# Optimization experiments

Measured on AMD Instinct MI355X. Metric: run time of the kernel, lower is better.

Reference implementation:

```python
import jax, jax.numpy as jnp
import numpy as np

B, C, E = 4, 2048, 1024
H, D = 16, 64

def setup_inputs() -> dict:
    key = jax.random.key(0)
    kx, kq, kk, kv, ko = jax.random.split(key, 5)
    s = 1.0 / np.sqrt(E)
    return {
        "x": jax.random.normal(kx, (B, C, E), dtype=jnp.float32),
        "W_q": jax.random.uniform(kq, (E, H * D), jnp.float32, -s, s),
        "W_k": jax.random.uniform(kk, (E, H * D), jnp.float32, -s, s),
        "W_v": jax.random.uniform(kv, (E, H * D), jnp.float32, -s, s),
        "W_o": jax.random.uniform(ko, (H * D, E), jnp.float32, -s, s),
    }

def reference(x, W_q, W_k, W_v, W_o):
    b, c, e = x.shape
    # project and split heads: [B, H, C, D]
    q = (x @ W_q).reshape(b, c, H, D).transpose(0, 2, 1, 3)
    k = (x @ W_k).reshape(b, c, H, D).transpose(0, 2, 1, 3)
    v = (x @ W_v).reshape(b, c, H, D).transpose(0, 2, 1, 3)
    scores = jnp.einsum('bhqd,bhkd->bhqk', q, k) / jnp.sqrt(jnp.float32(D))
    causal = jnp.tril(jnp.ones((c, c), dtype=bool))
    scores = jnp.where(causal, scores, -jnp.inf)
    weights = jax.nn.softmax(scores, axis=-1)
    hidden = jnp.einsum('bhqk,bhkd->bhqd', weights, v)
    hidden = hidden.transpose(0, 2, 1, 3).reshape(b, c, H * D)
    return hidden @ W_o
```

## Files before the change

### kernel.cpp

```cpp
#include <hip/hip_runtime.h>
#include <hip/hip_bf16.h>


typedef __attribute__((ext_vector_type(8))) short short8;
typedef __attribute__((ext_vector_type(4))) float floatx4;
typedef __attribute__((ext_vector_type(4))) unsigned short ushort4v;

__device__ __forceinline__ unsigned short f2bf(float f) {
    __hip_bfloat16 h = __float2bfloat16(f);
    return __builtin_bit_cast(unsigned short, h);
}

__device__ __forceinline__ void gl2lds16(const unsigned short* g, unsigned short* l) {
    __builtin_amdgcn_global_load_lds(
        (const __attribute__((address_space(1))) unsigned int*)g,
        (__attribute__((address_space(3))) unsigned int*)l, 16, 0, 0);
}

__global__ __launch_bounds__(256) void prep_kernel(const float* __restrict__ x,
                                                   const float* __restrict__ W0,
                                                   const float* __restrict__ W1,
                                                   const float* __restrict__ W2,
                                                   const float* __restrict__ W3,
                                                   unsigned short* __restrict__ xb,
                                                   unsigned short* __restrict__ wt) {
    __shared__ float tile[64][65];
    const int id = blockIdx.x;
    if (id < 8192) {
        const int i = id * 256 + threadIdx.x;
        const float4 v = ((const float4*)x)[i];
        ushort4v o;
        o[0] = f2bf(v.x); o[1] = f2bf(v.y); o[2] = f2bf(v.z); o[3] = f2bf(v.w);
        ((ushort4v*)xb)[i] = o;
        return;
    }
    const int t2 = id - 8192;
    const int z = t2 >> 8;
    const float* src = (z == 0) ? W0 : (z == 1) ? W1 : (z == 2) ? W2 : W3;
    const float scale = (z == 0) ? 0.18033688011112042f : 1.0f;
    unsigned short* dst = wt + (size_t)z * 1048576;
    const int k0 = ((t2 >> 4) & 15) * 64, n0 = (t2 & 15) * 64;
    const int t = threadIdx.x;
    const int r = t >> 4, c4 = (t & 15) * 4;
    #pragma unroll
    for (int p = 0; p < 4; ++p) {
        const int kk = p * 16 + r;
        const float4 v = *(const float4*)&src[(size_t)(k0 + kk) * 1024 + n0 + c4];
        tile[kk][c4 + 0] = v.x; tile[kk][c4 + 1] = v.y;
        tile[kk][c4 + 2] = v.z; tile[kk][c4 + 3] = v.w;
    }
    __syncthreads();
    #pragma unroll
    for (int p = 0; p < 4; ++p) {
        const int nn = p * 16 + r;
        ushort4v o;
        #pragma unroll
        for (int j = 0; j < 4; ++j) o[j] = f2bf(tile[c4 + j][nn] * scale);
        *(ushort4v*)&dst[(size_t)(n0 + nn) * 1024 + k0 + c4] = o;
    }
}

template<int MODE, int NBLK>
__global__ __launch_bounds__(256) void gemm128(const unsigned short* __restrict__ A,
                                               const unsigned short* __restrict__ Bt,
                                               unsigned short* __restrict__ obf,
                                               float* __restrict__ ofp) {
    constexpr int Kd = 1024;
    __shared__ __align__(16) unsigned short Al[128 * 64];
    __shared__ __align__(16) unsigned short Bl[128 * 64];
    const int id = blockIdx.x;
    const int xcd = id & 7;
    const int q = id >> 3;
    const int m_blk = xcd * 8 + (q & 7);
    const int n_blk = q >> 3;
    const int m0 = m_blk * 128, n0 = n_blk * 128;

    const int tid = threadIdx.x;
    const int lane = tid & 63, w = tid >> 6;
    const int quad = lane >> 4, l15 = lane & 15;
    const int wm = (w & 1) * 64, wn = (w >> 1) * 64;
    const int srow = lane >> 3, sc = lane & 7;
    const int gc = (sc ^ srow) * 8;

    floatx4 acc[4][4];
    #pragma unroll
    for (int i = 0; i < 4; ++i)
        #pragma unroll
        for (int j = 0; j < 4; ++j) acc[i][j] = (floatx4){0.f, 0.f, 0.f, 0.f};

    for (int kt = 0; kt < Kd / 64; ++kt) {
        const int k0 = kt * 64;
        #pragma unroll
        for (int p = 0; p < 4; ++p) {
            const int row0 = w * 32 + p * 8;
            gl2lds16(&A[(size_t)(m0 + row0 + srow) * Kd + k0 + gc], &Al[row0 * 64]);
            gl2lds16(&Bt[(size_t)(n0 + row0 + srow) * Kd + k0 + gc], &Bl[row0 * 64]);
        }
        __syncthreads();
        #pragma unroll
        for (int kk = 0; kk < 2; ++kk) {
            short8 af[4], bfv[4];
            #pragma unroll
            for (int i = 0; i < 4; ++i) {
                const int row = wm + i * 16 + l15;
                af[i] = *(const short8*)&Al[row * 64 + ((kk * 4 + quad) ^ (row & 7)) * 8];
            }
            #pragma unroll
            for (int i = 0; i < 4; ++i) {
                const int row = wn + i * 16 + l15;
                bfv[i] = *(const short8*)&Bl[row * 64 + ((kk * 4 + quad) ^ (row & 7)) * 8];
            }
            #pragma unroll
            for (int i = 0; i < 4; ++i)
                #pragma unroll
                for (int j = 0; j < 4; ++j)
                    acc[i][j] = __builtin_amdgcn_mfma_f32_16x16x32_bf16(
                        af[i], bfv[j], acc[i][j], 0, 0, 0);
        }
        __syncthreads();
    }

    #pragma unroll
    for (int i = 0; i < 4; ++i) {
        if (MODE == 0 && n0 >= 2048) {
            #pragma unroll
            for (int j = 0; j < 4; ++j) {
                const int mb = m0 + wm + i * 16 + quad * 4;
                const int n = n0 + wn + j * 16 + l15;
                const int b = mb >> 11, c0 = mb & 2047;
                const int nl = n & 1023, hh = nl >> 6, d = nl & 63;
                ushort4v pv;
                #pragma unroll
                for (int r = 0; r < 4; ++r) pv[r] = f2bf(acc[i][j][r]);
                *(ushort4v*)&obf[16777216 + ((size_t)(b * 16 + hh) * 64 + d) * 2048 + c0] = pv;
            }
        } else {
            #pragma unroll
            for (int r = 0; r < 4; ++r) {
                const int m = m0 + wm + i * 16 + quad * 4 + r;
                #pragma unroll
                for (int j = 0; j < 4; ++j) {
                    const int n = n0 + wn + j * 16 + l15;
                    const float v = acc[i][j][r];
                    if (MODE == 0) {
                        const int b = m >> 11, c = m & 2047;
                        const int z = n >> 10, nl = n & 1023, hh = nl >> 6, d = nl & 63;
                        obf[(size_t)z * 8388608 +
                            ((size_t)(b * 16 + hh) * 2048 + c) * 64 + d] = f2bf(v);
                    } else {
                        ofp[(size_t)m * 1024 + n] = v;
                    }
                }
            }
        }
    }
}

__global__ __launch_bounds__(512) void attn_kernel(const unsigned short* __restrict__ Q,
                                                   const unsigned short* __restrict__ K,
                                                   const unsigned short* __restrict__ Vt,
                                                   unsigned short* __restrict__ Hid) {
    __shared__ __align__(16) unsigned short Kl[2][64 * 64];
    __shared__ __align__(16) unsigned short Vl[2][64 * 64];
    __shared__ __align__(16) unsigned short Pl[8][16 * 72];
    const int id = blockIdx.x;
    const int bh = (id >> 6) * 8 + (id & 7);
    const int xq = (id >> 3) & 7;
    const int b = bh >> 4, h = bh & 15;
    const int tid = threadIdx.x, w = tid >> 6, lane = tid & 63;
    const int quad = lane >> 4, l15 = lane & 15;
    const int sw = quad ^ (l15 & 7);
    const int srow = lane >> 3, sc = lane & 7;
    const int g8 = (sc ^ srow) * 8;
    const int krow = w * 8 + srow;
    const size_t bhs = (size_t)(b * 16 + h) * 2048 * 64;
    const unsigned short* Qb = Q + bhs;
    const unsigned short* Kb = K + bhs;
    const unsigned short* Vb = Vt + bhs;

    #pragma unroll
    for (int pass = 0; pass < 2; ++pass) {
        const int qt = pass ? (15 - xq) : xq;
        const int q0 = qt * 128;
        const int qw = q0 + w * 16;
        const int myq = qw + l15;
        const short8 bq0 = *(const short8*)&Qb[(size_t)myq * 64 + quad * 8];
        const short8 bq1 = *(const short8*)&Qb[(size_t)myq * 64 + 32 + quad * 8];

        floatx4 o[4];
        #pragma unroll
        for (int i = 0; i < 4; ++i) o[i] = (floatx4){0.f, 0.f, 0.f, 0.f};
        float li = 0.f;

        const int nT = (q0 + 128) >> 6;
        __syncthreads();
        gl2lds16(&Kb[(size_t)krow * 64 + g8], &Kl[0][w * 512]);
        gl2lds16(&Vb[(size_t)krow * 2048 + g8], &Vl[0][w * 512]);

        for (int t = 0; t < nT; ++t) {
            const int k0 = t * 64;
            const int cb = t & 1;
            __syncthreads();
            if (t + 1 < nT) {
                const int kn = k0 + 64;
                gl2lds16(&Kb[(size_t)(kn + krow) * 64 + g8], &Kl[cb ^ 1][w * 512]);
                gl2lds16(&Vb[(size_t)krow * 2048 + kn + g8], &Vl[cb ^ 1][w * 512]);
            }
            if (k0 <= qw + 15) {
                floatx4 s[4];
                #pragma unroll
                for (int kf = 0; kf < 4; ++kf) {
                    const int row = kf * 16 + l15;
                    const short8 ka0 = *(const short8*)&Kl[cb][row * 64 + sw * 8];
                    const short8 ka1 = *(const short8*)&Kl[cb][row * 64 + (sw ^ 4) * 8];
                    floatx4 ss = (floatx4){0.f, 0.f, 0.f, 0.f};
                    ss = __builtin_amdgcn_mfma_f32_16x16x32_bf16(ka0, bq0, ss, 0, 0, 0);
                    ss = __builtin_amdgcn_mfma_f32_16x16x32_bf16(ka1, bq1, ss, 0, 0, 0);
                    s[kf] = ss;
                }
                if (k0 + 63 > qw) {
                    #pragma unroll
                    for (int kf = 0; kf < 4; ++kf) {
                        ushort4v pw;
                        #pragma unroll
                        for (int r = 0; r < 4; ++r) {
                            const int key = k0 + kf * 16 + quad * 4 + r;
                            const float p = (key > myq) ? 0.f
                                            : __builtin_amdgcn_exp2f(s[kf][r]);
                            li += p;
                            pw[r] = f2bf(p);
                        }
                        *(ushort4v*)&Pl[w][l15 * 72 + kf * 16 + quad * 4] = pw;
                    }
                } else {
                    #pragma unroll
                    for (int kf = 0; kf < 4; ++kf) {
                        ushort4v pw;
                        #pragma unroll
                        for (int r = 0; r < 4; ++r) {
                            const float p = __builtin_amdgcn_exp2f(s[kf][r]);
                            li += p;
                            pw[r] = f2bf(p);
                        }
                        *(ushort4v*)&Pl[w][l15 * 72 + kf * 16 + quad * 4] = pw;
                    }
                }
                __threadfence_block();
                const short8 pb0 = *(const short8*)&Pl[w][l15 * 72 + quad * 8];
                const short8 pb1 = *(const short8*)&Pl[w][l15 * 72 + 32 + quad * 8];
                #pragma unroll
                for (int nt = 0; nt < 4; ++nt) {
                    const int row = nt * 16 + l15;
                    const short8 va0 = *(const short8*)&Vl[cb][row * 64 + sw * 8];
                    const short8 va1 = *(const short8*)&Vl[cb][row * 64 + (sw ^ 4) * 8];
                    floatx4 oo = o[nt];
                    oo = __builtin_amdgcn_mfma_f32_16x16x32_bf16(va0, pb0, oo, 0, 0, 0);
                    oo = __builtin_amdgcn_mfma_f32_16x16x32_bf16(va1, pb1, oo, 0, 0, 0);
                    o[nt] = oo;
                }
            }
        }

        li += __shfl_xor(li, 16, 64);
        li += __shfl_xor(li, 32, 64);
        const float inv = 1.f / li;
        #pragma unroll
        for (int nt = 0; nt < 4; ++nt) {
            ushort4v ov;
            #pragma unroll
            for (int r = 0; r < 4; ++r) ov[r] = f2bf(o[nt][r] * inv);
            *(ushort4v*)&Hid[((size_t)b * 2048 + myq) * 1024 + h * 64 + nt * 16 + quad * 4] = ov;
        }
    }
}

extern "C" void kernel_launch(void* const* d_in, const int* in_sizes, int n_in,
                              void* d_out, int out_size, void* d_ws, size_t ws_size,
                              hipStream_t stream) {
    const float* x  = (const float*)d_in[0];
    const float* Wq = (const float*)d_in[1];
    const float* Wk = (const float*)d_in[2];
    const float* Wv = (const float*)d_in[3];
    const float* Wo = (const float*)d_in[4];
    float* out = (float*)d_out;
    unsigned short* ws = (unsigned short*)d_ws;

    const size_t XB  = 0;
    const size_t WQT = 8388608;
    const size_t QO  = 12582912;
    const size_t HO  = 37748736;

    prep_kernel<<<9216, 256, 0, stream>>>(x, Wq, Wk, Wv, Wo, ws + XB, ws + WQT);

    gemm128<0, 24><<<1536, 256, 0, stream>>>(ws + XB, ws + WQT, ws + QO, nullptr);
    attn_kernel<<<512, 512, 0, stream>>>(ws + QO, ws + QO + 8388608,
                                         ws + QO + 16777216, ws + HO);
    gemm128<1, 8><<<512, 256, 0, stream>>>(ws + HO, ws + WQT + 3145728, nullptr, out);
}
```

Measured before the change: 232.9 us.

## Use 256x256 double-buffered tiles for the QKV projection GEMM

Replaces the 128x128 QKV GEMM with a dedicated 512-thread kernel that computes 256x256 output tiles, with 8 waves each holding 128x64 accumulators. It double-buffers the LDS tiles so the next K-slice loads while MFMAs run on the current one, with one barrier per step. The larger tile raises arithmetic intensity and cuts global traffic, and the prefetch hides load latency. In exchange it uses more registers and 128KB of LDS per block, and launches only 384 blocks, which may leave CUs underused. The output projection is split into its own specialised kernel without the mode template.

```diff
diff --git a/kernel.cpp b/kernel.cpp
--- a/kernel.cpp
+++ b/kernel.cpp
@@ -60,11 +60,110 @@
     }
 }
 
-template<int MODE, int NBLK>
-__global__ __launch_bounds__(256) void gemm128(const unsigned short* __restrict__ A,
-                                               const unsigned short* __restrict__ Bt,
-                                               unsigned short* __restrict__ obf,
-                                               float* __restrict__ ofp) {
+__global__ __launch_bounds__(512, 2) void gemmqkv(const unsigned short* __restrict__ A,
+                                                  const unsigned short* __restrict__ Bt,
+                                                  unsigned short* __restrict__ obf) {
+    constexpr int Kd = 1024;
+    __shared__ __align__(16) unsigned short Al[2][256 * 64];
+    __shared__ __align__(16) unsigned short Bl[2][256 * 64];
+    const int id = blockIdx.x;
+    const int xcd = id & 7;
+    const int idx = id >> 3;
+    const int m_blk = xcd * 4 + (idx & 3);
+    const int n_blk = idx >> 2;
+    const int m0 = m_blk * 256, n0 = n_blk * 256;
+
+    const int tid = threadIdx.x;
+    const int lane = tid & 63, w = tid >> 6;
+    const int quad = lane >> 4, l15 = lane & 15;
+    const int wm = (w & 1) * 128, wn = (w >> 1) * 64;
+    const int srow = lane >> 3, sc = lane & 7;
+    const int gc = (sc ^ srow) * 8;
+
+    floatx4 acc[8][4];
+    #pragma unroll
+    for (int i = 0; i < 8; ++i)
+        #pragma unroll
+        for (int j = 0; j < 4; ++j) acc[i][j] = (floatx4){0.f, 0.f, 0.f, 0.f};
+
+    #pragma unroll
+    for (int p = 0; p < 4; ++p) {
+        const int row0 = w * 32 + p * 8;
+        gl2lds16(&A[(size_t)(m0 + row0 + srow) * Kd + gc], &Al[0][row0 * 64]);
+        gl2lds16(&Bt[(size_t)(n0 + row0 + srow) * Kd + gc], &Bl[0][row0 * 64]);
+    }
+
+    for (int kt = 0; kt < 16; ++kt) {
+        const int cb = kt & 1;
+        __syncthreads();
+        if (kt < 15) {
+            const int kn = kt * 64 + 64;
+            #pragma unroll
+            for (int p = 0; p < 4; ++p) {
+                const int row0 = w * 32 + p * 8;
+                gl2lds16(&A[(size_t)(m0 + row0 + srow) * Kd + kn + gc],
+                         &Al[cb ^ 1][row0 * 64]);
+                gl2lds16(&Bt[(size_t)(n0 + row0 + srow) * Kd + kn + gc],
+                         &Bl[cb ^ 1][row0 * 64]);
+            }
+        }
+        #pragma unroll
+        for (int kk = 0; kk < 2; ++kk) {
+            short8 af[8], bfv[4];
+            #pragma unroll
+            for (int j = 0; j < 4; ++j) {
+                const int row = wn + j * 16 + l15;
+                bfv[j] = *(const short8*)&Bl[cb][row * 64 + ((kk * 4 + quad) ^ (row & 7)) * 8];
+            }
+            #pragma unroll
+            for (int i = 0; i < 8; ++i) {
+                const int row = wm + i * 16 + l15;
+                af[i] = *(const short8*)&Al[cb][row * 64 + ((kk * 4 + quad) ^ (row & 7)) * 8];
+            }
+            #pragma unroll
+            for (int i = 0; i < 8; ++i)
+                #pragma unroll
+                for (int j = 0; j < 4; ++j)
+                    acc[i][j] = __builtin_amdgcn_mfma_f32_16x16x32_bf16(
+                        af[i], bfv[j], acc[i][j], 0, 0, 0);
+        }
+    }
+
+    if (n0 >= 2048) {
+        #pragma unroll
+        for (int i = 0; i < 8; ++i)
+            #pragma unroll
+            for (int j = 0; j < 4; ++j) {
+                const int mb = m0 + wm + i * 16 + quad * 4;
+                const int n = n0 + wn + j * 16 + l15;
+                const int b = mb >> 11, c0 = mb & 2047;
+                const int nl = n & 1023, hh = nl >> 6, d = nl & 63;
+                ushort4v pv;
+                #pragma unroll
+                for (int r = 0; r < 4; ++r) pv[r] = f2bf(acc[i][j][r]);
+                *(ushort4v*)&obf[16777216 + ((size_t)(b * 16 + hh) * 64 + d) * 2048 + c0] = pv;
+            }
+    } else {
+        #pragma unroll
+        for (int i = 0; i < 8; ++i)
+            #pragma unroll
+            for (int r = 0; r < 4; ++r) {
+                const int m = m0 + wm + i * 16 + quad * 4 + r;
+                const int b = m >> 11, c = m & 2047;
+                #pragma unroll
+                for (int j = 0; j < 4; ++j) {
+                    const int n = n0 + wn + j * 16 + l15;
+                    const int z = n >> 10, nl = n & 1023, hh = nl >> 6, d = nl & 63;
+                    obf[(size_t)z * 8388608 +
+                        ((size_t)(b * 16 + hh) * 2048 + c) * 64 + d] = f2bf(acc[i][j][r]);
+                }
+            }
+    }
+}
+
+__global__ __launch_bounds__(256) void gemmproj(const unsigned short* __restrict__ A,
+                                                const unsigned short* __restrict__ Bt,
+                                                float* __restrict__ ofp) {
     constexpr int Kd = 1024;
     __shared__ __align__(16) unsigned short Al[128 * 64];
     __shared__ __align__(16) unsigned short Bl[128 * 64];
@@ -121,39 +220,14 @@
     }
 
     #pragma unroll
-    for (int i = 0; i < 4; ++i) {
-        if (MODE == 0 && n0 >= 2048) {
-            #pragma unroll
-            for (int j = 0; j < 4; ++j) {
-                const int mb = m0 + wm + i * 16 + quad * 4;
-                const int n = n0 + wn + j * 16 + l15;
-                const int b = mb >> 11, c0 = mb & 2047;
-                const int nl = n & 1023, hh = nl >> 6, d = nl & 63;
-                ushort4v pv;
-                #pragma unroll
-                for (int r = 0; r < 4; ++r) pv[r] = f2bf(acc[i][j][r]);
-                *(ushort4v*)&obf[16777216 + ((size_t)(b * 16 + hh) * 64 + d) * 2048 + c0] = pv;
-            }
-        } else {
-            #pragma unroll
-            for (int r = 0; r < 4; ++r) {
-                const int m = m0 + wm + i * 16 + quad * 4 + r;
-                #pragma unroll
-                for (int j = 0; j < 4; ++j) {
-                    const int n = n0 + wn + j * 16 + l15;
-                    const float v = acc[i][j][r];
-                    if (MODE == 0) {
-                        const int b = m >> 11, c = m & 2047;
-                        const int z = n >> 10, nl = n & 1023, hh = nl >> 6, d = nl & 63;
-                        obf[(size_t)z * 8388608 +
-                            ((size_t)(b * 16 + hh) * 2048 + c) * 64 + d] = f2bf(v);
-                    } else {
-                        ofp[(size_t)m * 1024 + n] = v;
-                    }
-                }
-            }
-        }
-    }
+    for (int i = 0; i < 4; ++i)
+        #pragma unroll
+        for (int r = 0; r < 4; ++r) {
+            const int m = m0 + wm + i * 16 + quad * 4 + r;
+            #pragma unroll
+            for (int j = 0; j < 4; ++j)
+                ofp[(size_t)m * 1024 + n0 + wn + j * 16 + l15] = acc[i][j][r];
+        }
 }
 
 __global__ __launch_bounds__(512) void attn_kernel(const unsigned short* __restrict__ Q,
@@ -292,8 +366,8 @@
 
     prep_kernel<<<9216, 256, 0, stream>>>(x, Wq, Wk, Wv, Wo, ws + XB, ws + WQT);
 
-    gemm128<0, 24><<<1536, 256, 0, stream>>>(ws + XB, ws + WQT, ws + QO, nullptr);
+    gemmqkv<<<384, 512, 0, stream>>>(ws + XB, ws + WQT, ws + QO);
     attn_kernel<<<512, 512, 0, stream>>>(ws + QO, ws + QO + 8388608,
                                          ws + QO + 16777216, ws + HO);
-    gemm128<1, 8><<<512, 256, 0, stream>>>(ws + HO, ws + WQT + 3145728, nullptr, out);
-}
+    gemmproj<<<512, 256, 0, stream>>>(ws + HO, ws + WQT + 3145728, out);
+}
```

Result: slower. 250.1 us (+7.4%).
